# Optimization experiments

Hardware: AMD Instinct MI355X
Metric: run time of the kernel (lower is better)

The kernel has to match this reference:

```python
import jax, jax.numpy as jnp
import numpy as np
import math

TAU = 2.0
EPS = 1e-5
ALPHA = 2.0  # spikingjelly surrogate.ATan default alpha

@jax.custom_vjp
def atan_spike(x):
    return (x >= 0.0).astype(x.dtype)

def _spike_fwd(x):
    return atan_spike(x), x

def _spike_bwd(x, g):
    s = math.pi / 2.0 * ALPHA
    return (g * (ALPHA / 2.0) / (1.0 + (s * x) ** 2),)

atan_spike.defvjp(_spike_fwd, _spike_bwd)

def lif_seq(x_seq):
    # MultiStepLIFNode: v' = v + (x - v)/tau ; spike = H(v'-1) ; hard reset to v_reset=0
    def step(v, x):
        v = v + (x - v) / TAU
        s = atan_spike(v - 1.0)
        v = v * (1.0 - jax.lax.stop_gradient(s))  # detach_reset=True
        return v, s
    _, s_seq = jax.lax.scan(step, jnp.zeros_like(x_seq[0]), x_seq)
    return s_seq

def setup_inputs() -> dict:
    key = jax.random.key(0)
    kx, kw = jax.random.split(key)
    T, B, N, P, D = 4, 64, 1024, 63, 128
    x = jax.random.normal(kx, (T, B, N, P), dtype=jnp.float32)
    W = jax.random.normal(kw, (D, P), dtype=jnp.float32) * np.float32(1.0 / np.sqrt(P))
    gamma = jnp.ones((D,), dtype=jnp.float32)
    beta = jnp.zeros((D,), dtype=jnp.float32)
    return {"x": x, "W": W, "gamma": gamma, "beta": beta, "pe": 0}

def reference(x, W, gamma, beta, pe):
    # bias-free Linear: [T,B,N,P] x [D,P] -> [T,B,N,D]
    h = jnp.einsum('tbnp,dp->tbnd', x, W)
    # BatchNorm1d over channel D; training-mode batch stats over (T*B, N)
    mean = jnp.mean(h, axis=(0, 1, 2), keepdims=True)
    var = jnp.var(h, axis=(0, 1, 2), keepdims=True)  # biased, as torch BN normalization
    h = (h - mean) * jax.lax.rsqrt(var + EPS) * gamma + beta
    # multi-step LIF across T (self.pe=False -> tAPE branch skipped)
    out = lif_seq(h)  # [T,B,N,D] == original output after final transpose
    return out
```

## Files before the change

### kernel.cpp

```cpp
#include <hip/hip_runtime.h>
#include <math.h>

#define T_STEPS 4
#define R_ROWS  65536
#define M_ROWS  262144
#define P_DIM   63
#define D_DIM   128
#define PP      64

#define TILES_TOTAL (M_ROWS / 64)
#define G_CHUNKS 8

typedef float v4f __attribute__((ext_vector_type(4)));

__global__ __launch_bounds__(256) void gram_kernel(const float* __restrict__ x,
                                                   double* __restrict__ partials,
                                                   int tiles_per_block) {
    __shared__ __align__(16) float xt[2][64 * PP];
    const int tid = threadIdx.x;
    const int tj = tid & 15;
    const int ti = tid >> 4;

    double dacc[4][4];
#pragma unroll
    for (int a = 0; a < 4; a++)
#pragma unroll
        for (int b = 0; b < 4; b++) dacc[a][b] = 0.0;

    if (tid < 64) {
        xt[0][tid * PP + 63] = 1.0f;
        xt[1][tid * PP + 63] = 1.0f;
    }

    const int tile0 = blockIdx.x * tiles_per_block;
    float4 reg[4];

    {
        const float4* src = (const float4*)(x + (size_t)tile0 * (64 * 63));
#pragma unroll
        for (int it = 0; it < 4; it++) {
            int k = tid + it * 256;
            reg[it] = (k < 1008) ? src[k] : make_float4(0.f, 0.f, 0.f, 0.f);
        }
    }
#pragma unroll
    for (int it = 0; it < 4; it++) {
        int k = tid + it * 256;
        if (k < 1008) {
            const float* ve = (const float*)&reg[it];
            int flat = k * 4;
#pragma unroll
            for (int e = 0; e < 4; e++) {
                int f = flat + e;
                int r = f / 63;
                int c = f - r * 63;
                xt[0][r * PP + c] = ve[e];
            }
        }
    }
    __syncthreads();

    for (int t = 0; t < tiles_per_block; t++) {
        const int cur = t & 1;
        if (t + 1 < tiles_per_block) {
            const float4* src = (const float4*)(x + (size_t)(tile0 + t + 1) * (64 * 63));
#pragma unroll
            for (int it = 0; it < 4; it++) {
                int k = tid + it * 256;
                reg[it] = (k < 1008) ? src[k] : make_float4(0.f, 0.f, 0.f, 0.f);
            }
        }

        float facc[4][4];
#pragma unroll
        for (int a = 0; a < 4; a++)
#pragma unroll
            for (int b = 0; b < 4; b++) facc[a][b] = 0.0f;

        const float* buf = xt[cur];
        for (int r = 0; r < 64; r++) {
            float4 xi = *(const float4*)&buf[r * PP + ti * 4];
            float4 xj = *(const float4*)&buf[r * PP + tj * 4];
            const float* xia = (const float*)&xi;
            const float* xja = (const float*)&xj;
#pragma unroll
            for (int a = 0; a < 4; a++)
#pragma unroll
                for (int b = 0; b < 4; b++)
                    facc[a][b] = fmaf(xia[a], xja[b], facc[a][b]);
        }
#pragma unroll
        for (int a = 0; a < 4; a++)
#pragma unroll
            for (int b = 0; b < 4; b++) dacc[a][b] += (double)facc[a][b];

        __syncthreads();
        if (t + 1 < tiles_per_block) {
            float* nbuf = xt[1 - cur];
#pragma unroll
            for (int it = 0; it < 4; it++) {
                int k = tid + it * 256;
                if (k < 1008) {
                    const float* ve = (const float*)&reg[it];
                    int flat = k * 4;
#pragma unroll
                    for (int e = 0; e < 4; e++) {
                        int f = flat + e;
                        int r = f / 63;
                        int c = f - r * 63;
                        nbuf[r * PP + c] = ve[e];
                    }
                }
            }
            __syncthreads();
        }
    }

    double* Pb = partials + (size_t)blockIdx.x * 4096;
#pragma unroll
    for (int a = 0; a < 4; a++)
#pragma unroll
        for (int b = 0; b < 4; b++)
            Pb[(ti * 4 + a) * 64 + (tj * 4 + b)] = dacc[a][b];
}

__global__ __launch_bounds__(256) void reduce_kernel(const double* __restrict__ partials,
                                                     double* __restrict__ G8,
                                                     const float* __restrict__ W,
                                                     float* __restrict__ Wt,
                                                     int copies_per_chunk) {
    if (blockIdx.x >= G_CHUNKS * 16) {
        int widx = (blockIdx.x - G_CHUNKS * 16) * 256 + threadIdx.x;
        for (int j = widx; j < P_DIM * D_DIM; j += 8 * 256) {
            int p = j >> 7;
            int d = j & 127;
            Wt[j] = W[d * P_DIM + p];
        }
        return;
    }
    const int chunk = blockIdx.x >> 4;
    const int idx   = (blockIdx.x & 15) * 256 + threadIdx.x;
    const double* src = partials + (size_t)chunk * copies_per_chunk * 4096;
    double s = 0.0;
    for (int c = 0; c < copies_per_chunk; c++)
        s += src[(size_t)c * 4096 + idx];
    G8[(size_t)chunk * 4096 + idx] = s;
}

__global__ __launch_bounds__(64) void stats_kernel(const double* __restrict__ G,
                                                   const float* __restrict__ W,
                                                   const float* __restrict__ gamma,
                                                   const float* __restrict__ beta,
                                                   float* __restrict__ stats) {
    const int d = blockIdx.x;
    const int p = threadIdx.x;
    __shared__ float sW[64];
    sW[p] = (p < P_DIM) ? W[d * P_DIM + p] : 0.0f;
    __syncthreads();

    double inner = 0.0;
#pragma unroll
    for (int c = 0; c < G_CHUNKS; c++) {
        const double* Gr = G + (size_t)c * (64 * 64) + p * 64;
        for (int q = 0; q < 64; q++) inner += Gr[q] * (double)sW[q];
    }

    double contrib = (double)sW[p] * inner;
    double ex2M = contrib;
#pragma unroll
    for (int off = 32; off > 0; off >>= 1) ex2M += __shfl_down(ex2M, off, 64);
    double meanM = __shfl(inner, 63, 64);

    if (p == 0) {
        double mean = meanM / (double)M_ROWS;
        double ex2  = ex2M  / (double)M_ROWS;
        double var  = ex2 - mean * mean;
        float varf  = (float)var;
        float vpe   = varf + 1e-5f;
        float invstd = (float)(1.0 / sqrt((double)vpe));
        stats[d * 4 + 0] = (float)mean;
        stats[d * 4 + 1] = invstd;
        stats[d * 4 + 2] = gamma[d];
        stats[d * 4 + 3] = beta[d];
    }
}

#define LIF_ROWS 16
#define SX_STRIDE 64
__global__ __launch_bounds__(256) void lif_kernel(const float* __restrict__ x,
                                                  const float* __restrict__ Wt,
                                                  const float* __restrict__ stats,
                                                  float* __restrict__ out) {
    __shared__ __align__(16) float sw[P_DIM * D_DIM];
    __shared__ __align__(16) float sx[T_STEPS * LIF_ROWS * SX_STRIDE];
    const int tid = threadIdx.x;

    {
        const float4* wt4 = (const float4*)Wt;
        float4* sw4 = (float4*)sw;
#pragma unroll
        for (int i = 0; i < 8; i++) {
            int k = tid + i * 256;
            if (k < 2016) sw4[k] = wt4[k];
        }
    }

    const int r0 = blockIdx.x * LIF_ROWS;
    const int seg = tid >> 6;
    const int lane = tid & 63;
    const v4f* src = (const v4f*)(x + ((size_t)seg * R_ROWS + r0) * P_DIM);
#pragma unroll
    for (int kk = 0; kk < 4; kk++) {
        int k = lane + kk * 64;
        v4f v;
        if (k < 252) v = __builtin_nontemporal_load(&src[k]);
        if (k < 252) {
            int flat = k * 4;
#pragma unroll
            for (int e = 0; e < 4; e++) {
                int f = flat + e;
                int r = f / 63;
                int c = f - r * 63;
                sx[(seg * LIF_ROWS + r) * SX_STRIDE + c] = v[e];
            }
        }
    }
    __syncthreads();

    const int td = tid & 31;
    const int tr = tid >> 5;
    const int d0 = td * 4;
    const int rowa = tr * 2;

    float acc[8][4];
#pragma unroll
    for (int u = 0; u < 8; u++)
#pragma unroll
        for (int j = 0; j < 4; j++) acc[u][j] = 0.0f;

#pragma unroll
    for (int pq = 0; pq < 15; pq++) {
        const int p = pq * 4;
        float4 w0 = *(const float4*)&sw[(p + 0) * D_DIM + d0];
        float4 w1 = *(const float4*)&sw[(p + 1) * D_DIM + d0];
        float4 w2 = *(const float4*)&sw[(p + 2) * D_DIM + d0];
        float4 w3 = *(const float4*)&sw[(p + 3) * D_DIM + d0];
#pragma unroll
        for (int t = 0; t < T_STEPS; t++)
#pragma unroll
            for (int i = 0; i < 2; i++) {
                float4 xv = *(const float4*)&sx[(t * LIF_ROWS + rowa + i) * SX_STRIDE + p];
                float* a = acc[t * 2 + i];
                a[0] = fmaf(xv.x, w0.x, a[0]);
                a[1] = fmaf(xv.x, w0.y, a[1]);
                a[2] = fmaf(xv.x, w0.z, a[2]);
                a[3] = fmaf(xv.x, w0.w, a[3]);
                a[0] = fmaf(xv.y, w1.x, a[0]);
                a[1] = fmaf(xv.y, w1.y, a[1]);
                a[2] = fmaf(xv.y, w1.z, a[2]);
                a[3] = fmaf(xv.y, w1.w, a[3]);
                a[0] = fmaf(xv.z, w2.x, a[0]);
                a[1] = fmaf(xv.z, w2.y, a[1]);
                a[2] = fmaf(xv.z, w2.z, a[2]);
                a[3] = fmaf(xv.z, w2.w, a[3]);
                a[0] = fmaf(xv.w, w3.x, a[0]);
                a[1] = fmaf(xv.w, w3.y, a[1]);
                a[2] = fmaf(xv.w, w3.z, a[2]);
                a[3] = fmaf(xv.w, w3.w, a[3]);
            }
    }
#pragma unroll
    for (int p = 60; p < 63; p++) {
        float4 w4 = *(const float4*)&sw[p * D_DIM + d0];
#pragma unroll
        for (int t = 0; t < T_STEPS; t++)
#pragma unroll
            for (int i = 0; i < 2; i++) {
                float xv = sx[(t * LIF_ROWS + rowa + i) * SX_STRIDE + p];
                float* a = acc[t * 2 + i];
                a[0] = fmaf(xv, w4.x, a[0]);
                a[1] = fmaf(xv, w4.y, a[1]);
                a[2] = fmaf(xv, w4.z, a[2]);
                a[3] = fmaf(xv, w4.w, a[3]);
            }
    }

#pragma unroll
    for (int i = 0; i < 2; i++) {
        const int row = r0 + rowa + i;
        float sval[T_STEPS][4];
#pragma unroll
        for (int j = 0; j < 4; j++) {
            float4 st = ((const float4*)stats)[d0 + j];
            float v = 0.0f;
#pragma unroll
            for (int t = 0; t < T_STEPS; t++) {
                float hn = (acc[t * 2 + i][j] - st.x) * st.y;
                hn = hn * st.z;
                hn = hn + st.w;
                v = v + (hn - v) * 0.5f;
                float s = (v >= 1.0f) ? 1.0f : 0.0f;
                sval[t][j] = s;
                if (s != 0.0f) v = 0.0f;
            }
        }
#pragma unroll
        for (int t = 0; t < T_STEPS; t++) {
            v4f o = {sval[t][0], sval[t][1], sval[t][2], sval[t][3]};
            __builtin_nontemporal_store(
                o, (v4f*)&out[((size_t)t * R_ROWS + row) * D_DIM + d0]);
        }
    }
}

extern "C" void kernel_launch(void* const* d_in, const int* in_sizes, int n_in,
                              void* d_out, int out_size, void* d_ws, size_t ws_size,
                              hipStream_t stream) {
    const float* x     = (const float*)d_in[0];
    const float* W     = (const float*)d_in[1];
    const float* gamma = (const float*)d_in[2];
    const float* beta  = (const float*)d_in[3];
    float* out = (float*)d_out;

    const size_t fixed = (size_t)G_CHUNKS * 4096 * 8 + 2048 + 32768 + 4096;
    int nparts = 512;
    while (nparts > 64 && (size_t)nparts * 4096 * 8 + fixed > ws_size) nparts >>= 1;
    const int tiles_per_block = TILES_TOTAL / nparts;

    double* partials = (double*)d_ws;
    double* G8       = (double*)((char*)d_ws + (size_t)nparts * 4096 * 8);
    float*  stats    = (float*)((char*)G8 + (size_t)G_CHUNKS * 4096 * 8);
    float*  Wt       = (float*)((char*)stats + 2048);

    gram_kernel<<<nparts, 256, 0, stream>>>(x, partials, tiles_per_block);
    reduce_kernel<<<G_CHUNKS * 16 + 8, 256, 0, stream>>>(partials, G8, W, Wt,
                                                         nparts / G_CHUNKS);
    stats_kernel<<<D_DIM, 64, 0, stream>>>(G8, W, gamma, beta, stats);
    lif_kernel<<<R_ROWS / LIF_ROWS, 256, 0, stream>>>(x, Wt, stats, out);
}
```

Measured before the change: 282.8 us.

## Double LIF block rows and widen per-thread column tile to eight

The LIF/GEMM kernel processes 32 rows per block instead of 16, and each thread now computes 8 output columns, giving an 8x8 accumulator tile. This amortises the per-block load of the full weight matrix into shared memory over more rows and raises FMA reuse per shared-memory read. It costs more registers and LDS per block, and adds a launch-bounds occupancy hint that may force spills or reduce the number of resident waves.

```diff
diff --git a/kernel.cpp b/kernel.cpp
--- a/kernel.cpp
+++ b/kernel.cpp
@@ -185,12 +185,12 @@
     }
 }
 
-#define LIF_ROWS 16
+#define LIF_ROWS 32
 #define SX_STRIDE 64
-__global__ __launch_bounds__(256) void lif_kernel(const float* __restrict__ x,
-                                                  const float* __restrict__ Wt,
-                                                  const float* __restrict__ stats,
-                                                  float* __restrict__ out) {
+__global__ __launch_bounds__(256, 2) void lif_kernel(const float* __restrict__ x,
+                                                     const float* __restrict__ Wt,
+                                                     const float* __restrict__ stats,
+                                                     float* __restrict__ out) {
     __shared__ __align__(16) float sw[P_DIM * D_DIM];
     __shared__ __align__(16) float sx[T_STEPS * LIF_ROWS * SX_STRIDE];
     const int tid = threadIdx.x;
@@ -210,11 +210,11 @@
     const int lane = tid & 63;
     const v4f* src = (const v4f*)(x + ((size_t)seg * R_ROWS + r0) * P_DIM);
 #pragma unroll
-    for (int kk = 0; kk < 4; kk++) {
+    for (int kk = 0; kk < 8; kk++) {
         int k = lane + kk * 64;
         v4f v;
-        if (k < 252) v = __builtin_nontemporal_load(&src[k]);
-        if (k < 252) {
+        if (k < 504) v = __builtin_nontemporal_load(&src[k]);
+        if (k < 504) {
             int flat = k * 4;
 #pragma unroll
             for (int e = 0; e < 4; e++) {
@@ -227,70 +227,73 @@
     }
     __syncthreads();
 
-    const int td = tid & 31;
-    const int tr = tid >> 5;
-    const int d0 = td * 4;
+    const int td = tid & 15;
+    const int tr = tid >> 4;
+    const int d0 = td * 8;
     const int rowa = tr * 2;
 
-    float acc[8][4];
+    float acc[8][8];
 #pragma unroll
     for (int u = 0; u < 8; u++)
 #pragma unroll
-        for (int j = 0; j < 4; j++) acc[u][j] = 0.0f;
+        for (int j = 0; j < 8; j++) acc[u][j] = 0.0f;
 
 #pragma unroll
     for (int pq = 0; pq < 15; pq++) {
         const int p = pq * 4;
-        float4 w0 = *(const float4*)&sw[(p + 0) * D_DIM + d0];
-        float4 w1 = *(const float4*)&sw[(p + 1) * D_DIM + d0];
-        float4 w2 = *(const float4*)&sw[(p + 2) * D_DIM + d0];
-        float4 w3 = *(const float4*)&sw[(p + 3) * D_DIM + d0];
+        float4 wa[4], wb[4];
+#pragma unroll
+        for (int pp = 0; pp < 4; pp++) {
+            wa[pp] = *(const float4*)&sw[(p + pp) * D_DIM + d0];
+            wb[pp] = *(const float4*)&sw[(p + pp) * D_DIM + d0 + 4];
+        }
 #pragma unroll
         for (int t = 0; t < T_STEPS; t++)
 #pragma unroll
             for (int i = 0; i < 2; i++) {
                 float4 xv = *(const float4*)&sx[(t * LIF_ROWS + rowa + i) * SX_STRIDE + p];
+                const float xs[4] = {xv.x, xv.y, xv.z, xv.w};
                 float* a = acc[t * 2 + i];
-                a[0] = fmaf(xv.x, w0.x, a[0]);
-                a[1] = fmaf(xv.x, w0.y, a[1]);
-                a[2] = fmaf(xv.x, w0.z, a[2]);
-                a[3] = fmaf(xv.x, w0.w, a[3]);
-                a[0] = fmaf(xv.y, w1.x, a[0]);
-                a[1] = fmaf(xv.y, w1.y, a[1]);
-                a[2] = fmaf(xv.y, w1.z, a[2]);
-                a[3] = fmaf(xv.y, w1.w, a[3]);
-                a[0] = fmaf(xv.z, w2.x, a[0]);
-                a[1] = fmaf(xv.z, w2.y, a[1]);
-                a[2] = fmaf(xv.z, w2.z, a[2]);
-                a[3] = fmaf(xv.z, w2.w, a[3]);
-                a[0] = fmaf(xv.w, w3.x, a[0]);
-                a[1] = fmaf(xv.w, w3.y, a[1]);
-                a[2] = fmaf(xv.w, w3.z, a[2]);
-                a[3] = fmaf(xv.w, w3.w, a[3]);
+#pragma unroll
+                for (int pp = 0; pp < 4; pp++) {
+                    a[0] = fmaf(xs[pp], wa[pp].x, a[0]);
+                    a[1] = fmaf(xs[pp], wa[pp].y, a[1]);
+                    a[2] = fmaf(xs[pp], wa[pp].z, a[2]);
+                    a[3] = fmaf(xs[pp], wa[pp].w, a[3]);
+                    a[4] = fmaf(xs[pp], wb[pp].x, a[4]);
+                    a[5] = fmaf(xs[pp], wb[pp].y, a[5]);
+                    a[6] = fmaf(xs[pp], wb[pp].z, a[6]);
+                    a[7] = fmaf(xs[pp], wb[pp].w, a[7]);
+                }
             }
     }
 #pragma unroll
     for (int p = 60; p < 63; p++) {
-        float4 w4 = *(const float4*)&sw[p * D_DIM + d0];
+        float4 wa = *(const float4*)&sw[p * D_DIM + d0];
+        float4 wb = *(const float4*)&sw[p * D_DIM + d0 + 4];
 #pragma unroll
         for (int t = 0; t < T_STEPS; t++)
 #pragma unroll
             for (int i = 0; i < 2; i++) {
                 float xv = sx[(t * LIF_ROWS + rowa + i) * SX_STRIDE + p];
                 float* a = acc[t * 2 + i];
-                a[0] = fmaf(xv, w4.x, a[0]);
-                a[1] = fmaf(xv, w4.y, a[1]);
-                a[2] = fmaf(xv, w4.z, a[2]);
-                a[3] = fmaf(xv, w4.w, a[3]);
+                a[0] = fmaf(xv, wa.x, a[0]);
+                a[1] = fmaf(xv, wa.y, a[1]);
+                a[2] = fmaf(xv, wa.z, a[2]);
+                a[3] = fmaf(xv, wa.w, a[3]);
+                a[4] = fmaf(xv, wb.x, a[4]);
+                a[5] = fmaf(xv, wb.y, a[5]);
+                a[6] = fmaf(xv, wb.z, a[6]);
+                a[7] = fmaf(xv, wb.w, a[7]);
             }
     }
 
 #pragma unroll
     for (int i = 0; i < 2; i++) {
         const int row = r0 + rowa + i;
-        float sval[T_STEPS][4];
-#pragma unroll
-        for (int j = 0; j < 4; j++) {
+        float sval[T_STEPS][8];
+#pragma unroll
+        for (int j = 0; j < 8; j++) {
             float4 st = ((const float4*)stats)[d0 + j];
             float v = 0.0f;
 #pragma unroll
@@ -306,9 +309,12 @@
         }
 #pragma unroll
         for (int t = 0; t < T_STEPS; t++) {
-            v4f o = {sval[t][0], sval[t][1], sval[t][2], sval[t][3]};
+            v4f o0 = {sval[t][0], sval[t][1], sval[t][2], sval[t][3]};
+            v4f o1 = {sval[t][4], sval[t][5], sval[t][6], sval[t][7]};
             __builtin_nontemporal_store(
-                o, (v4f*)&out[((size_t)t * R_ROWS + row) * D_DIM + d0]);
+                o0, (v4f*)&out[((size_t)t * R_ROWS + row) * D_DIM + d0]);
+            __builtin_nontemporal_store(
+                o1, (v4f*)&out[((size_t)t * R_ROWS + row) * D_DIM + d0 + 4]);
         }
     }
 }
```

Result: slower. 300.2 us (+6.1%).

## Retile LIF GEMM: 64 rows per block, wave-uniform weight loads, swizzled LDS

Applied to the files above, without the earlier changes.

The LIF kernel now handles 64 rows per block instead of 16. Each wave owns 32 output channels, and each lane owns one row across all 4 timesteps, so every lane keeps 128 accumulators. Weights are padded to 64 columns and read directly from global memory at wave-uniform addresses, which lets them go through scalar or broadcast loads instead of being staged through shared memory. The x tile in LDS uses an XOR swizzle to avoid bank conflicts. The large register footprint may limit occupancy, and output stores are now strided per lane by row, which may hurt write coalescing.

```diff
diff --git a/kernel.cpp b/kernel.cpp
--- a/kernel.cpp
+++ b/kernel.cpp
@@ -127,14 +127,14 @@
 __global__ __launch_bounds__(256) void reduce_kernel(const double* __restrict__ partials,
                                                      double* __restrict__ G8,
                                                      const float* __restrict__ W,
-                                                     float* __restrict__ Wt,
+                                                     float* __restrict__ Wp,
                                                      int copies_per_chunk) {
     if (blockIdx.x >= G_CHUNKS * 16) {
         int widx = (blockIdx.x - G_CHUNKS * 16) * 256 + threadIdx.x;
-        for (int j = widx; j < P_DIM * D_DIM; j += 8 * 256) {
-            int p = j >> 7;
-            int d = j & 127;
-            Wt[j] = W[d * P_DIM + p];
+        for (int j = widx; j < D_DIM * 64; j += 8 * 256) {
+            int d = j >> 6;
+            int p = j & 63;
+            Wp[j] = (p < P_DIM) ? W[d * P_DIM + p] : 0.0f;
         }
         return;
     }
@@ -185,131 +185,95 @@
     }
 }
 
-#define LIF_ROWS 16
-#define SX_STRIDE 64
-__global__ __launch_bounds__(256) void lif_kernel(const float* __restrict__ x,
-                                                  const float* __restrict__ Wt,
-                                                  const float* __restrict__ stats,
-                                                  float* __restrict__ out) {
-    __shared__ __align__(16) float sw[P_DIM * D_DIM];
-    __shared__ __align__(16) float sx[T_STEPS * LIF_ROWS * SX_STRIDE];
+__global__ __launch_bounds__(256, 2) void lif_kernel(const float* __restrict__ x,
+                                                     const float* __restrict__ Wp,
+                                                     const float* __restrict__ stats,
+                                                     float* __restrict__ out) {
+    __shared__ __align__(16) float sx[T_STEPS * 64 * 64];
     const int tid = threadIdx.x;
-
-    {
-        const float4* wt4 = (const float4*)Wt;
-        float4* sw4 = (float4*)sw;
-#pragma unroll
-        for (int i = 0; i < 8; i++) {
-            int k = tid + i * 256;
-            if (k < 2016) sw4[k] = wt4[k];
-        }
-    }
-
-    const int r0 = blockIdx.x * LIF_ROWS;
     const int seg = tid >> 6;
     const int lane = tid & 63;
+
+    sx[(seg * 64 + lane) * 64 + (((15 ^ (lane & 7)) << 2) | 3)] = 0.0f;
+
+    const int r0 = blockIdx.x * 64;
     const v4f* src = (const v4f*)(x + ((size_t)seg * R_ROWS + r0) * P_DIM);
 #pragma unroll
-    for (int kk = 0; kk < 4; kk++) {
+    for (int kk = 0; kk < 16; kk++) {
         int k = lane + kk * 64;
         v4f v;
-        if (k < 252) v = __builtin_nontemporal_load(&src[k]);
-        if (k < 252) {
+        if (k < 1008) v = __builtin_nontemporal_load(&src[k]);
+        if (k < 1008) {
             int flat = k * 4;
 #pragma unroll
             for (int e = 0; e < 4; e++) {
                 int f = flat + e;
                 int r = f / 63;
                 int c = f - r * 63;
-                sx[(seg * LIF_ROWS + r) * SX_STRIDE + c] = v[e];
+                sx[(seg * 64 + r) * 64 + ((((c >> 2) ^ (r & 7)) << 2) | (c & 3))] = v[e];
             }
         }
     }
     __syncthreads();
 
-    const int td = tid & 31;
-    const int tr = tid >> 5;
-    const int d0 = td * 4;
-    const int rowa = tr * 2;
-
-    float acc[8][4];
-#pragma unroll
-    for (int u = 0; u < 8; u++)
-#pragma unroll
-        for (int j = 0; j < 4; j++) acc[u][j] = 0.0f;
-
-#pragma unroll
-    for (int pq = 0; pq < 15; pq++) {
-        const int p = pq * 4;
-        float4 w0 = *(const float4*)&sw[(p + 0) * D_DIM + d0];
-        float4 w1 = *(const float4*)&sw[(p + 1) * D_DIM + d0];
-        float4 w2 = *(const float4*)&sw[(p + 2) * D_DIM + d0];
-        float4 w3 = *(const float4*)&sw[(p + 3) * D_DIM + d0];
+    const int wv = __builtin_amdgcn_readfirstlane(tid >> 6);
+    const int d0 = wv * 32;
+    const float* __restrict__ wbase = Wp + (size_t)d0 * 64;
+    const int s7 = lane & 7;
+
+    float acc[T_STEPS][32];
+#pragma unroll
+    for (int t = 0; t < T_STEPS; t++)
+#pragma unroll
+        for (int c = 0; c < 32; c++) acc[t][c] = 0.0f;
+
+#pragma unroll 2
+    for (int pq = 0; pq < 16; pq++) {
+        float4 xq[T_STEPS];
 #pragma unroll
         for (int t = 0; t < T_STEPS; t++)
-#pragma unroll
-            for (int i = 0; i < 2; i++) {
-                float4 xv = *(const float4*)&sx[(t * LIF_ROWS + rowa + i) * SX_STRIDE + p];
-                float* a = acc[t * 2 + i];
-                a[0] = fmaf(xv.x, w0.x, a[0]);
-                a[1] = fmaf(xv.x, w0.y, a[1]);
-                a[2] = fmaf(xv.x, w0.z, a[2]);
-                a[3] = fmaf(xv.x, w0.w, a[3]);
-                a[0] = fmaf(xv.y, w1.x, a[0]);
-                a[1] = fmaf(xv.y, w1.y, a[1]);
-                a[2] = fmaf(xv.y, w1.z, a[2]);
-                a[3] = fmaf(xv.y, w1.w, a[3]);
-                a[0] = fmaf(xv.z, w2.x, a[0]);
-                a[1] = fmaf(xv.z, w2.y, a[1]);
-                a[2] = fmaf(xv.z, w2.z, a[2]);
-                a[3] = fmaf(xv.z, w2.w, a[3]);
-                a[0] = fmaf(xv.w, w3.x, a[0]);
-                a[1] = fmaf(xv.w, w3.y, a[1]);
-                a[2] = fmaf(xv.w, w3.z, a[2]);
-                a[3] = fmaf(xv.w, w3.w, a[3]);
-            }
-    }
-#pragma unroll
-    for (int p = 60; p < 63; p++) {
-        float4 w4 = *(const float4*)&sw[p * D_DIM + d0];
-#pragma unroll
-        for (int t = 0; t < T_STEPS; t++)
-#pragma unroll
-            for (int i = 0; i < 2; i++) {
-                float xv = sx[(t * LIF_ROWS + rowa + i) * SX_STRIDE + p];
-                float* a = acc[t * 2 + i];
-                a[0] = fmaf(xv, w4.x, a[0]);
-                a[1] = fmaf(xv, w4.y, a[1]);
-                a[2] = fmaf(xv, w4.z, a[2]);
-                a[3] = fmaf(xv, w4.w, a[3]);
-            }
-    }
-
-#pragma unroll
-    for (int i = 0; i < 2; i++) {
-        const int row = r0 + rowa + i;
-        float sval[T_STEPS][4];
-#pragma unroll
-        for (int j = 0; j < 4; j++) {
-            float4 st = ((const float4*)stats)[d0 + j];
+            xq[t] = *(const float4*)&sx[(t * 64 + lane) * 64 + ((pq ^ s7) << 2)];
+
+#pragma unroll
+        for (int c = 0; c < 32; c++) {
+            float4 w = *(const float4*)&wbase[c * 64 + (pq << 2)];
+            const float* wa = (const float*)&w;
+#pragma unroll
+            for (int pp = 0; pp < 4; pp++) {
+                const float wval = wa[pp];
+#pragma unroll
+                for (int t = 0; t < T_STEPS; t++) {
+                    const float xval = ((const float*)&xq[t])[pp];
+                    acc[t][c] = fmaf(xval, wval, acc[t][c]);
+                }
+            }
+        }
+    }
+
+    const int rowg = r0 + lane;
+#pragma unroll
+    for (int jq = 0; jq < 8; jq++) {
+        v4f o[T_STEPS];
+#pragma unroll
+        for (int j4 = 0; j4 < 4; j4++) {
+            const int c = jq * 4 + j4;
+            float4 st = ((const float4*)stats)[d0 + c];
             float v = 0.0f;
 #pragma unroll
             for (int t = 0; t < T_STEPS; t++) {
-                float hn = (acc[t * 2 + i][j] - st.x) * st.y;
+                float hn = (acc[t][c] - st.x) * st.y;
                 hn = hn * st.z;
                 hn = hn + st.w;
                 v = v + (hn - v) * 0.5f;
                 float s = (v >= 1.0f) ? 1.0f : 0.0f;
-                sval[t][j] = s;
+                o[t][j4] = s;
                 if (s != 0.0f) v = 0.0f;
             }
         }
 #pragma unroll
-        for (int t = 0; t < T_STEPS; t++) {
-            v4f o = {sval[t][0], sval[t][1], sval[t][2], sval[t][3]};
+        for (int t = 0; t < T_STEPS; t++)
             __builtin_nontemporal_store(
-                o, (v4f*)&out[((size_t)t * R_ROWS + row) * D_DIM + d0]);
-        }
+                o[t], (v4f*)&out[((size_t)t * R_ROWS + rowg) * D_DIM + d0 + jq * 4]);
     }
 }
 
@@ -330,11 +294,11 @@
     double* partials = (double*)d_ws;
     double* G8       = (double*)((char*)d_ws + (size_t)nparts * 4096 * 8);
     float*  stats    = (float*)((char*)G8 + (size_t)G_CHUNKS * 4096 * 8);
-    float*  Wt       = (float*)((char*)stats + 2048);
+    float*  Wp       = (float*)((char*)stats + 2048);
 
     gram_kernel<<<nparts, 256, 0, stream>>>(x, partials, tiles_per_block);
-    reduce_kernel<<<G_CHUNKS * 16 + 8, 256, 0, stream>>>(partials, G8, W, Wt,
+    reduce_kernel<<<G_CHUNKS * 16 + 8, 256, 0, stream>>>(partials, G8, W, Wp,
                                                          nparts / G_CHUNKS);
     stats_kernel<<<D_DIM, 64, 0, stream>>>(G8, W, gamma, beta, stats);
-    lif_kernel<<<R_ROWS / LIF_ROWS, 256, 0, stream>>>(x, Wt, stats, out);
-}
+    lif_kernel<<<R_ROWS / 64, 256, 0, stream>>>(x, Wp, stats, out);
+}
```

Result: slower. 591.2 us (+109.0%).

## Split LIF kernel across two D-halves per row tile to cut LDS and registers

Applied to the files above, without the earlier changes.

Each LIF block now computes only 64 of the 128 output channels for its 16-row tile, with twice as many blocks launched. The per-block weight tile in shared memory halves and each thread keeps 4 timesteps × 4 channels of accumulators instead of 8×4, which should raise occupancy. In exchange, every x tile is loaded from global memory twice, once per half, adding read traffic to a kernel that is likely memory-bound.

```diff
diff --git a/kernel.cpp b/kernel.cpp
--- a/kernel.cpp
+++ b/kernel.cpp
@@ -191,21 +191,26 @@
                                                   const float* __restrict__ Wt,
                                                   const float* __restrict__ stats,
                                                   float* __restrict__ out) {
-    __shared__ __align__(16) float sw[P_DIM * D_DIM];
+    __shared__ __align__(16) float sw[P_DIM * 64];
     __shared__ __align__(16) float sx[T_STEPS * LIF_ROWS * SX_STRIDE];
     const int tid = threadIdx.x;
+    const int half = blockIdx.x & 1;
+    const int r0 = (blockIdx.x >> 1) * LIF_ROWS;
 
     {
         const float4* wt4 = (const float4*)Wt;
         float4* sw4 = (float4*)sw;
-#pragma unroll
-        for (int i = 0; i < 8; i++) {
-            int k = tid + i * 256;
-            if (k < 2016) sw4[k] = wt4[k];
-        }
-    }
-
-    const int r0 = blockIdx.x * LIF_ROWS;
+        const int hbase = half * 16;
+#pragma unroll
+        for (int i = 0; i < 4; i++) {
+            int j = tid + i * 256;
+            if (j < 1008) {
+                int p = j >> 4, cq = j & 15;
+                sw4[j] = wt4[p * 32 + hbase + cq];
+            }
+        }
+    }
+
     const int seg = tid >> 6;
     const int lane = tid & 63;
     const v4f* src = (const v4f*)(x + ((size_t)seg * R_ROWS + r0) * P_DIM);
@@ -227,89 +232,85 @@
     }
     __syncthreads();
 
-    const int td = tid & 31;
-    const int tr = tid >> 5;
-    const int d0 = td * 4;
-    const int rowa = tr * 2;
-
-    float acc[8][4];
-#pragma unroll
-    for (int u = 0; u < 8; u++)
-#pragma unroll
-        for (int j = 0; j < 4; j++) acc[u][j] = 0.0f;
+    const int td = tid & 15;
+    const int tr = tid >> 4;
+    const int dl = td * 4;
+
+    float acc[T_STEPS][4];
+#pragma unroll
+    for (int t = 0; t < T_STEPS; t++)
+#pragma unroll
+        for (int j = 0; j < 4; j++) acc[t][j] = 0.0f;
 
 #pragma unroll
     for (int pq = 0; pq < 15; pq++) {
         const int p = pq * 4;
-        float4 w0 = *(const float4*)&sw[(p + 0) * D_DIM + d0];
-        float4 w1 = *(const float4*)&sw[(p + 1) * D_DIM + d0];
-        float4 w2 = *(const float4*)&sw[(p + 2) * D_DIM + d0];
-        float4 w3 = *(const float4*)&sw[(p + 3) * D_DIM + d0];
+        float4 w0 = *(const float4*)&sw[(p + 0) * 64 + dl];
+        float4 w1 = *(const float4*)&sw[(p + 1) * 64 + dl];
+        float4 w2 = *(const float4*)&sw[(p + 2) * 64 + dl];
+        float4 w3 = *(const float4*)&sw[(p + 3) * 64 + dl];
+        float4 xv[T_STEPS];
 #pragma unroll
         for (int t = 0; t < T_STEPS; t++)
-#pragma unroll
-            for (int i = 0; i < 2; i++) {
-                float4 xv = *(const float4*)&sx[(t * LIF_ROWS + rowa + i) * SX_STRIDE + p];
-                float* a = acc[t * 2 + i];
-                a[0] = fmaf(xv.x, w0.x, a[0]);
-                a[1] = fmaf(xv.x, w0.y, a[1]);
-                a[2] = fmaf(xv.x, w0.z, a[2]);
-                a[3] = fmaf(xv.x, w0.w, a[3]);
-                a[0] = fmaf(xv.y, w1.x, a[0]);
-                a[1] = fmaf(xv.y, w1.y, a[1]);
-                a[2] = fmaf(xv.y, w1.z, a[2]);
-                a[3] = fmaf(xv.y, w1.w, a[3]);
-                a[0] = fmaf(xv.z, w2.x, a[0]);
-                a[1] = fmaf(xv.z, w2.y, a[1]);
-                a[2] = fmaf(xv.z, w2.z, a[2]);
-                a[3] = fmaf(xv.z, w2.w, a[3]);
-                a[0] = fmaf(xv.w, w3.x, a[0]);
-                a[1] = fmaf(xv.w, w3.y, a[1]);
-                a[2] = fmaf(xv.w, w3.z, a[2]);
-                a[3] = fmaf(xv.w, w3.w, a[3]);
-            }
+            xv[t] = *(const float4*)&sx[(t * LIF_ROWS + tr) * SX_STRIDE + p];
+#pragma unroll
+        for (int t = 0; t < T_STEPS; t++) {
+            float* a = acc[t];
+            a[0] = fmaf(xv[t].x, w0.x, a[0]);
+            a[1] = fmaf(xv[t].x, w0.y, a[1]);
+            a[2] = fmaf(xv[t].x, w0.z, a[2]);
+            a[3] = fmaf(xv[t].x, w0.w, a[3]);
+            a[0] = fmaf(xv[t].y, w1.x, a[0]);
+            a[1] = fmaf(xv[t].y, w1.y, a[1]);
+            a[2] = fmaf(xv[t].y, w1.z, a[2]);
+            a[3] = fmaf(xv[t].y, w1.w, a[3]);
+            a[0] = fmaf(xv[t].z, w2.x, a[0]);
+            a[1] = fmaf(xv[t].z, w2.y, a[1]);
+            a[2] = fmaf(xv[t].z, w2.z, a[2]);
+            a[3] = fmaf(xv[t].z, w2.w, a[3]);
+            a[0] = fmaf(xv[t].w, w3.x, a[0]);
+            a[1] = fmaf(xv[t].w, w3.y, a[1]);
+            a[2] = fmaf(xv[t].w, w3.z, a[2]);
+            a[3] = fmaf(xv[t].w, w3.w, a[3]);
+        }
     }
 #pragma unroll
     for (int p = 60; p < 63; p++) {
-        float4 w4 = *(const float4*)&sw[p * D_DIM + d0];
-#pragma unroll
-        for (int t = 0; t < T_STEPS; t++)
-#pragma unroll
-            for (int i = 0; i < 2; i++) {
-                float xv = sx[(t * LIF_ROWS + rowa + i) * SX_STRIDE + p];
-                float* a = acc[t * 2 + i];
-                a[0] = fmaf(xv, w4.x, a[0]);
-                a[1] = fmaf(xv, w4.y, a[1]);
-                a[2] = fmaf(xv, w4.z, a[2]);
-                a[3] = fmaf(xv, w4.w, a[3]);
-            }
-    }
-
-#pragma unroll
-    for (int i = 0; i < 2; i++) {
-        const int row = r0 + rowa + i;
-        float sval[T_STEPS][4];
-#pragma unroll
-        for (int j = 0; j < 4; j++) {
-            float4 st = ((const float4*)stats)[d0 + j];
-            float v = 0.0f;
-#pragma unroll
-            for (int t = 0; t < T_STEPS; t++) {
-                float hn = (acc[t * 2 + i][j] - st.x) * st.y;
-                hn = hn * st.z;
-                hn = hn + st.w;
-                v = v + (hn - v) * 0.5f;
-                float s = (v >= 1.0f) ? 1.0f : 0.0f;
-                sval[t][j] = s;
-                if (s != 0.0f) v = 0.0f;
-            }
-        }
+        float4 w4 = *(const float4*)&sw[p * 64 + dl];
 #pragma unroll
         for (int t = 0; t < T_STEPS; t++) {
-            v4f o = {sval[t][0], sval[t][1], sval[t][2], sval[t][3]};
-            __builtin_nontemporal_store(
-                o, (v4f*)&out[((size_t)t * R_ROWS + row) * D_DIM + d0]);
-        }
+            float xvs = sx[(t * LIF_ROWS + tr) * SX_STRIDE + p];
+            float* a = acc[t];
+            a[0] = fmaf(xvs, w4.x, a[0]);
+            a[1] = fmaf(xvs, w4.y, a[1]);
+            a[2] = fmaf(xvs, w4.z, a[2]);
+            a[3] = fmaf(xvs, w4.w, a[3]);
+        }
+    }
+
+    const int row = r0 + tr;
+    const int dg = half * 64 + dl;
+    float sval[T_STEPS][4];
+#pragma unroll
+    for (int j = 0; j < 4; j++) {
+        float4 st = ((const float4*)stats)[dg + j];
+        float v = 0.0f;
+#pragma unroll
+        for (int t = 0; t < T_STEPS; t++) {
+            float hn = (acc[t][j] - st.x) * st.y;
+            hn = hn * st.z;
+            hn = hn + st.w;
+            v = v + (hn - v) * 0.5f;
+            float s = (v >= 1.0f) ? 1.0f : 0.0f;
+            sval[t][j] = s;
+            if (s != 0.0f) v = 0.0f;
+        }
+    }
+#pragma unroll
+    for (int t = 0; t < T_STEPS; t++) {
+        v4f o = {sval[t][0], sval[t][1], sval[t][2], sval[t][3]};
+        __builtin_nontemporal_store(
+            o, (v4f*)&out[((size_t)t * R_ROWS + row) * D_DIM + dg]);
     }
 }
 
@@ -336,5 +337,5 @@
     reduce_kernel<<<G_CHUNKS * 16 + 8, 256, 0, stream>>>(partials, G8, W, Wt,
                                                          nparts / G_CHUNKS);
     stats_kernel<<<D_DIM, 64, 0, stream>>>(G8, W, gamma, beta, stats);
-    lif_kernel<<<R_ROWS / LIF_ROWS, 256, 0, stream>>>(x, Wt, stats, out);
-}
+    lif_kernel<<<R_ROWS / LIF_ROWS * 2, 256, 0, stream>>>(x, Wt, stats, out);
+}
```

Result: slower. 304.6 us (+7.7%).
